# Performance work log

Hardware: AMD Instinct MI355X
Metric: run time of the kernel (lower is better)

## Reference

```python
import jax, jax.numpy as jnp
import numpy as np

D_MODEL = 1024
NUM_HEADS = 16
D_K = D_MODEL // NUM_HEADS
B, S = 2, 2048
LN_EPS = 1e-5


def setup_inputs() -> dict:
    key = jax.random.key(0)
    ks = jax.random.split(key, 11)
    sc = 1.0 / np.sqrt(D_MODEL)
    return {
        "x": jax.random.normal(ks[0], (B, S, D_MODEL), dtype=jnp.float32),
        "Wq": jax.random.normal(ks[1], (D_MODEL, D_MODEL), dtype=jnp.float32) * sc,
        "bq": jnp.zeros((D_MODEL,), dtype=jnp.float32),
        "Wk": jax.random.normal(ks[2], (D_MODEL, D_MODEL), dtype=jnp.float32) * sc,
        "bk": jnp.zeros((D_MODEL,), dtype=jnp.float32),
        "Wv": jax.random.normal(ks[3], (D_MODEL, D_MODEL), dtype=jnp.float32) * sc,
        "bv": jnp.zeros((D_MODEL,), dtype=jnp.float32),
        "Wo": jax.random.normal(ks[4], (D_MODEL, D_MODEL), dtype=jnp.float32) * sc,
        "bo": jnp.zeros((D_MODEL,), dtype=jnp.float32),
        "ln_gamma": jnp.ones((D_MODEL,), dtype=jnp.float32),
        "ln_beta": jnp.zeros((D_MODEL,), dtype=jnp.float32),
    }


def reference(x, Wq, bq, Wk, bk, Wv, bv, Wo, bo, ln_gamma, ln_beta):
    b, s, d = x.shape
    # QKV projections -> [B, H, S, D_K]
    def split_heads(y):
        return y.reshape(b, s, NUM_HEADS, D_K).transpose(0, 2, 1, 3)
    q = split_heads(x @ Wq + bq)
    k = split_heads(x @ Wk + bk)
    v = split_heads(x @ Wv + bv)
    # scores [B, H, S, S]; dropout is identity in eval mode
    scores = jnp.einsum("bhqd,bhkd->bhqk", q, k) / jnp.sqrt(jnp.float32(D_K))
    attn = jax.nn.softmax(scores, axis=-1)
    context = jnp.einsum("bhqk,bhkd->bhqd", attn, v)
    context = context.transpose(0, 2, 1, 3).reshape(b, s, d)
    out = context @ Wo + bo
    # residual + LayerNorm (eps=1e-5, torch default)
    h = x + out
    mu = jnp.mean(h, axis=-1, keepdims=True)
    var = jnp.var(h, axis=-1, keepdims=True)
    return (h - mu) / jnp.sqrt(var + LN_EPS) * ln_gamma + ln_beta
```

## Files before the change

kernel.cpp:

```cpp
#include <hip/hip_runtime.h>
#include <math.h>

#define D_MODEL 1024
#define NHEAD   16
#define DKK     64
#define BATCH   2
#define SEQ     2048
#define MROWS   (BATCH*SEQ)

typedef __attribute__((ext_vector_type(8)))  short bf16x8;
typedef __attribute__((ext_vector_type(4)))  short bf16x4;
typedef __attribute__((ext_vector_type(4)))  float f32x4;
typedef __attribute__((ext_vector_type(16))) float f32x16;

#define MFMA(a,b,c)   __builtin_amdgcn_mfma_f32_16x16x32_bf16((a),(b),(c),0,0,0)
#define MFMA32(a,b,c) __builtin_amdgcn_mfma_f32_32x32x16_bf16((a),(b),(c),0,0,0)

#define QSCALE 0.18033688f

#define SBAR() { __builtin_amdgcn_sched_barrier(0); \
                 __builtin_amdgcn_s_barrier();      \
                 __builtin_amdgcn_sched_barrier(0); }

#define CH  520
#define TIL (8*CH)

__device__ __forceinline__ short f2b(float f) {
    unsigned u = __float_as_uint(f);
    unsigned r = (u + 0x7FFFu + ((u >> 16) & 1u)) >> 16;
    return (short)r;
}
__device__ __forceinline__ float b2f(short s) {
    return __uint_as_float(((unsigned)(unsigned short)s) << 16);
}

__device__ __forceinline__ float fexp2(float x) {
    float r; asm("v_exp_f32 %0, %1" : "=v"(r) : "v"(x)); return r;
}

__device__ __forceinline__ void gld_lds16(const void* g, void* l) {
    __builtin_amdgcn_global_load_lds(
        (const __attribute__((address_space(1))) void*)g,
        (__attribute__((address_space(3))) void*)l, 16, 0, 0);
}

__global__ __launch_bounds__(256)
void prep_all(const float* __restrict__ x,
              const float* __restrict__ Wq, const float* __restrict__ Wk,
              const float* __restrict__ Wv, const float* __restrict__ Wo,
              short* __restrict__ xb, short* __restrict__ wt3,
              short* __restrict__ wot)
{
    const int z = blockIdx.z;
    if (z < 4) {
        const float* W = z==0 ? Wq : z==1 ? Wk : z==2 ? Wv : Wo;
        short* dst = (z < 3) ? (wt3 + (size_t)z*1024*1024) : wot;
        __shared__ float tile[32][33];
        const int tx = threadIdx.x & 31, ty = threadIdx.x >> 5;
        const int c0 = blockIdx.x*32, r0 = blockIdx.y*32;
        #pragma unroll
        for (int i = 0; i < 4; i++)
            tile[ty + i*8][tx] = W[(size_t)(r0 + ty + i*8)*1024 + c0 + tx];
        __syncthreads();
        #pragma unroll
        for (int i = 0; i < 4; i++)
            dst[(size_t)(c0 + ty + i*8)*1024 + r0 + tx] = f2b(tile[tx][ty + i*8]);
    } else {
        const int blk = (z-4)*1024 + blockIdx.y*32 + blockIdx.x;
        const int i = (blk*256 + threadIdx.x) * 8;
        float4 a = *(const float4*)(x + i);
        float4 c = *(const float4*)(x + i + 4);
        bf16x8 v;
        v[0]=f2b(a.x); v[1]=f2b(a.y); v[2]=f2b(a.z); v[3]=f2b(a.w);
        v[4]=f2b(c.x); v[5]=f2b(c.y); v[6]=f2b(c.z); v[7]=f2b(c.w);
        *(bf16x8*)(xb + i) = v;
    }
}

__global__ __launch_bounds__(512, 2)
void gemm_qkv(const short* __restrict__ A, const short* __restrict__ Bt,
              const float* __restrict__ bq, const float* __restrict__ bk,
              const float* __restrict__ bv,
              short* __restrict__ qb, short* __restrict__ kb, short* __restrict__ vtb)
{
    __shared__ short Ab[2*16384];
    __shared__ short Bb[2*12288];

    const int t = threadIdx.x;
    const int w = t >> 6, lane = t & 63;
    const int r = lane & 15, g4 = lane >> 4;
    const int wm = w >> 2, wn = w & 3;

    const int bid = blockIdx.x;
    const int xcd = bid & 7, idx = bid >> 3;
    const int mi  = (xcd >> 1) * 4 + (idx & 3);
    const int ni  = (xcd & 1) * 8 + (idx >> 2);
    const int m0 = mi * 256, n0 = ni * 192;

    const int srow = t >> 3;
    const int scol = ((t & 7) ^ (srow & 7)) * 8;

    f32x4 acc[8][3] = {};
    bf16x8 bfr[2][3];

#define QKV_STAGE(P, KT)                                                      \
    { const int kk = (KT) * 64 + scol;                                        \
      _Pragma("unroll")                                                       \
      for (int a = 0; a < 4; a++)                                             \
          gld_lds16(A + (size_t)(m0 + a*64 + srow)*1024 + kk,                 \
                    Ab + (P)*16384 + a*4096 + t*8);                           \
      _Pragma("unroll")                                                       \
      for (int p2 = 0; p2 < 3; p2++)                                          \
          gld_lds16(Bt + (size_t)(n0 + p2*64 + srow)*1024 + kk,               \
                    Bb + (P)*12288 + p2*4096 + t*8); }

#define QKV_PHASE2(P, MH)                                                     \
    { const short* Abase = Ab + (P)*16384 + wm*8192;                          \
      bf16x8 af[2][4];                                                        \
      _Pragma("unroll")                                                       \
      for (int ks = 0; ks < 2; ks++)                                          \
          _Pragma("unroll")                                                   \
          for (int i = 0; i < 4; i++)                                         \
              af[ks][i] = *(const bf16x8*)&Abase[((MH)*64 + i*16 + r)*64 +    \
                                                 ((ks*4 + g4) ^ (r&7))*8];    \
      if ((MH) == 0) {                                                        \
          const short* Bbase = Bb + (P)*12288;                                \
          _Pragma("unroll")                                                   \
          for (int ks = 0; ks < 2; ks++)                                      \
              _Pragma("unroll")                                               \
              for (int j = 0; j < 3; j++)                                     \
                  bfr[ks][j] = *(const bf16x8*)&Bbase[(wn*48 + j*16 + r)*64 + \
                                                      ((ks*4 + g4) ^ (r&7))*8]; \
      }                                                                       \
      __builtin_amdgcn_s_setprio(1);                                          \
      _Pragma("unroll")                                                       \
      for (int ks = 0; ks < 2; ks++)                                          \
          _Pragma("unroll")                                                   \
          for (int i = 0; i < 4; i++)                                         \
              _Pragma("unroll")                                               \
              for (int j = 0; j < 3; j++)                                     \
                  acc[(MH)*4+i][j] = MFMA(af[ks][i], bfr[ks][j],              \
                                          acc[(MH)*4+i][j]);                  \
      __builtin_amdgcn_s_setprio(0); }

    QKV_STAGE(0, 0)
    QKV_STAGE(1, 1)
    asm volatile("s_waitcnt vmcnt(7)" ::: "memory");
    __builtin_amdgcn_s_barrier();
    __builtin_amdgcn_sched_barrier(0);

    int p = 0;
    #pragma unroll 1
    for (int kt = 0; kt < 16; kt++) {
        QKV_PHASE2(p, 0)
        QKV_PHASE2(p, 1)
        SBAR();
        if (kt < 14) {
            QKV_STAGE(p, kt + 2)
            asm volatile("s_waitcnt vmcnt(7)" ::: "memory");
        } else {
            asm volatile("s_waitcnt vmcnt(0)" ::: "memory");
        }
        __builtin_amdgcn_s_barrier();
        __builtin_amdgcn_sched_barrier(0);
        p ^= 1;
    }
#undef QKV_STAGE
#undef QKV_PHASE2

    const int src4 = ((((lane & 3) << 4) | (lane >> 2)) << 2);
    const int dl   = lane >> 2;
    const int sl   = (lane & 3) * 4;

    #pragma unroll
    for (int n = 0; n < 3; n++) {
        const int colbase = n0 + wn*48 + n*16;
        const int proj    = colbase >> 10;
        const int within  = colbase & 1023;
        const int h       = within >> 6;
        const int d       = (within & 63) + r;
        const float* bias = (proj == 0) ? bq : (proj == 1) ? bk : bv;
        const float bval  = bias[within + r];
        #pragma unroll
        for (int m = 0; m < 8; m++) {
            const int growb = m0 + wm*128 + m*16 + g4*4;
            const int bidx  = growb >> 11;
            const int s     = growb & 2047;
            if (proj == 0) {
                #pragma unroll
                for (int i = 0; i < 4; i++)
                    qb[((size_t)(bidx*NHEAD + h)*SEQ + s + i)*DKK + d] =
                        f2b((acc[m][n][i] + bval) * QSCALE);
            } else if (proj == 1) {
                #pragma unroll
                for (int i = 0; i < 4; i++)
                    kb[((size_t)(bidx*NHEAD + h)*SEQ + s + i)*DKK + d] =
                        f2b(acc[m][n][i] + bval);
            } else {
                const int sbase = m0 + wm*128 + m*16;
                const int bidx2 = sbase >> 11;
                const int srw   = sbase & 2047;
                unsigned lo  = ((unsigned)(unsigned short)f2b(acc[m][n][1]+bval) << 16)
                             |  (unsigned)(unsigned short)f2b(acc[m][n][0]+bval);
                unsigned hi2 = ((unsigned)(unsigned short)f2b(acc[m][n][3]+bval) << 16)
                             |  (unsigned)(unsigned short)f2b(acc[m][n][2]+bval);
                unsigned t0 = (unsigned)__builtin_amdgcn_ds_bpermute(src4, (int)lo);
                unsigned t1 = (unsigned)__builtin_amdgcn_ds_bpermute(src4, (int)hi2);
                union { unsigned u[2]; bf16x4 v; } pk4;
                pk4.u[0] = t0; pk4.u[1] = t1;
                *(bf16x4*)(vtb + ((size_t)(bidx2*NHEAD + h)*DKK + (within & 63) + dl)*SEQ
                               + srw + sl) = pk4.v;
            }
        }
    }
}

__global__ __launch_bounds__(256)
void gemm_out(const short* __restrict__ A, const short* __restrict__ Bt,
              const float* __restrict__ bo, const short* __restrict__ resid,
              short* __restrict__ hb)
{
    __shared__ short As[2*128*32];
    __shared__ short Bs[2*64*32];
    const int t = threadIdx.x;
    const int w = t >> 6, lane = t & 63;
    const int r = lane & 15, g4 = lane >> 4;
    const int wr = w >> 1, wc = w & 1;

    const int bid = blockIdx.x;
    const int xcd = bid & 7, idx = bid >> 3;
    const int mi  = (xcd >> 1) * 8 + (idx & 7);
    const int ni  = (xcd & 1) * 8 + (idx >> 3);
    const int m0 = mi * 128, n0 = ni * 64;

    const int srow = lane >> 2, su = lane & 3;

    f32x4 acc[4][2] = {};

#define OUT_STAGE(BUF, K0)                                                     \
    { const int kk = (K0) & 1023;                                              \
      _Pragma("unroll")                                                        \
      for (int c = 0; c < 2; c++) {                                            \
          const int row = w*32 + c*16 + srow;                                  \
          gld_lds16(A + (size_t)(m0+row)*1024 + kk + 8*(su ^ ((row>>1)&3)),    \
                    As + (BUF)*4096 + w*1024 + c*512);                         \
      }                                                                        \
      { const int row = w*16 + srow;                                           \
        gld_lds16(Bt + (size_t)(n0+row)*1024 + kk + 8*(su ^ ((row>>1)&3)),     \
                  Bs + (BUF)*2048 + w*512); } }

    OUT_STAGE(0, 0)
    __syncthreads();

    int cur = 0;
    #pragma unroll 1
    for (int k0 = 0; k0 < 1024; k0 += 32) {
        OUT_STAGE(cur^1, k0 + 32)
        const short* Abase = As + cur*4096;
        const short* Bbase = Bs + cur*2048;
        bf16x8 af[4], bfr[2];
        #pragma unroll
        for (int m = 0; m < 4; m++) {
            const int row = wr*64 + m*16 + r;
            af[m] = *(const bf16x8*)&Abase[row*32 + (g4 ^ ((row>>1)&3))*8];
        }
        #pragma unroll
        for (int n = 0; n < 2; n++) {
            const int row = wc*32 + n*16 + r;
            bfr[n] = *(const bf16x8*)&Bbase[row*32 + (g4 ^ ((row>>1)&3))*8];
        }
        __builtin_amdgcn_s_setprio(1);
        #pragma unroll
        for (int m = 0; m < 4; m++)
            #pragma unroll
            for (int n = 0; n < 2; n++)
                acc[m][n] = MFMA(af[m], bfr[n], acc[m][n]);
        __builtin_amdgcn_s_setprio(0);
        __syncthreads();
        cur ^= 1;
    }
#undef OUT_STAGE

    #pragma unroll
    for (int n = 0; n < 2; n++) {
        const int col = n0 + wc*32 + n*16 + r;
        const float bval = bo[col];
        #pragma unroll
        for (int m = 0; m < 4; m++) {
            #pragma unroll
            for (int i = 0; i < 4; i++) {
                const int grow = m0 + wr*64 + m*16 + g4*4 + i;
                const size_t ofs = (size_t)grow*1024 + col;
                hb[ofs] = f2b(acc[m][n][i] + bval + b2f(resid[ofs]));
            }
        }
    }
}

__global__ __launch_bounds__(256, 2)
void attn_mfma(const short* __restrict__ Q, const short* __restrict__ K,
               const short* __restrict__ VT, short* __restrict__ ctx)
{
    __shared__ short Ks[4*TIL];
    __shared__ short Vs[4*TIL];

    const int t = threadIdx.x;
    const int w = t >> 6, lane = t & 63;
    const int l31 = lane & 31, hi = lane >> 5;
    const int srow8 = lane >> 3, su = lane & 7;
    const int lane8 = lane * 8;
    const int swz8  = (su ^ srow8) * 8;

    const int bid     = blockIdx.x;
    const int logical = (bid & 7) * 64 + (bid >> 3);
    const int bh_lin  = logical >> 4;
    const int qt      = logical & 15;
    const int b = bh_lin >> 4, h = bh_lin & 15;
    const int q0 = qt * 128 + w * 32;

    const size_t bh = (size_t)b * NHEAD + h;
    const short* Qp = Q  + bh * SEQ * DKK;
    const short* Kp = K  + bh * SEQ * DKK;
    const short* Vp = VT + bh * DKK * SEQ;

    const short* kstage = Kp + (size_t)(w*8 + srow8) * DKK + swz8;
    const short* vstage = Vp + (size_t)(w*8 + srow8) * SEQ + swz8;

    bf16x8 qf[4];
    #pragma unroll
    for (int d0 = 0; d0 < 4; d0++)
        qf[d0] = *(const bf16x8*)(Qp + (size_t)(q0 + l31)*DKK + d0*16 + hi*8);

    int koff[8], voff[8];
    #pragma unroll
    for (int i = 0; i < 8; i++) {
        const int kchunk = (i>>2)*4 + (l31>>3);
        koff[i] = kchunk*CH + (l31&7)*64 + ((((i&3)*2 + hi) ^ (l31&7)) * 8);
        const int vchunk = (i&1)*4 + (l31>>3);
        voff[i] = vchunk*CH + (l31&7)*64 + ((((i>>1)*2 + hi) ^ (l31&7)) * 8);
    }

    f32x16 o0A = {}, o1A = {}, o0B = {}, o1B = {}, lacc = {};

#define ATT_STAGE(KDST, VDST, J)                                               \
    { const size_t jj = (size_t)((J) & (SEQ-1));                               \
      const short* ksrc = kstage + jj*DKK;                                     \
      gld_lds16(ksrc,           (KDST) + w*CH + lane8);                        \
      gld_lds16(ksrc + 32*DKK,  (KDST) + (4+w)*CH + lane8);                    \
      const short* vsrc = vstage + jj;                                         \
      gld_lds16(vsrc,           (VDST) + w*CH + lane8);                        \
      gld_lds16(vsrc + 32*SEQ,  (VDST) + (4+w)*CH + lane8); }

#define QK_SUB(KB, S0, S1)                                                     \
    { bf16x8 kf[8];                                                            \
      _Pragma("unroll")                                                        \
      for (int i = 0; i < 8; i++) kf[i] = *(const bf16x8*)&(KB)[koff[i]];      \
      _Pragma("unroll")                                                        \
      for (int d0 = 0; d0 < 4; d0++) S0 = MFMA32(kf[d0],   qf[d0], S0);        \
      _Pragma("unroll")                                                        \
      for (int d0 = 0; d0 < 4; d0++) S1 = MFMA32(kf[4+d0], qf[d0], S1); }

#define PV_SUB(S0, S1, VB, O0, O1)                                             \
    { bf16x8 vf[8];                                                            \
      _Pragma("unroll")                                                        \
      for (int i = 0; i < 8; i++) vf[i] = *(const bf16x8*)&(VB)[voff[i]];      \
      _Pragma("unroll")                                                        \
      for (int ks = 0; ks < 4; ks++) {                                         \
        const int g = (ks & 1) * 8;                                            \
        float e0,e1,e2,e3,e4,e5,e6,e7;                                         \
        if (ks < 2) { e0=S0[g+0];e1=S0[g+1];e2=S0[g+2];e3=S0[g+3];             \
                      e4=S0[g+4];e5=S0[g+5];e6=S0[g+6];e7=S0[g+7]; }           \
        else        { e0=S1[g+0];e1=S1[g+1];e2=S1[g+2];e3=S1[g+3];             \
                      e4=S1[g+4];e5=S1[g+5];e6=S1[g+6];e7=S1[g+7]; }           \
        unsigned u0,u1,u2,u3;                                                  \
        asm("v_cvt_pk_bf16_f32 %0, %1, %2" : "=v"(u0) : "v"(e0), "v"(e1));     \
        asm("v_cvt_pk_bf16_f32 %0, %1, %2" : "=v"(u1) : "v"(e2), "v"(e3));     \
        asm("v_cvt_pk_bf16_f32 %0, %1, %2" : "=v"(u2) : "v"(e4), "v"(e5));     \
        asm("v_cvt_pk_bf16_f32 %0, %1, %2" : "=v"(u3) : "v"(e6), "v"(e7));     \
        auto rA = __builtin_amdgcn_permlane32_swap(u0, u2, false, false);      \
        auto rB = __builtin_amdgcn_permlane32_swap(u1, u3, false, false);      \
        union { unsigned u[4]; bf16x8 v; } pa;                                 \
        pa.u[0] = rA[0]; pa.u[1] = rB[0]; pa.u[2] = rA[1]; pa.u[3] = rB[1];    \
        O0 = MFMA32(pa.v, vf[ks*2+0], O0);                                     \
        O1 = MFMA32(pa.v, vf[ks*2+1], O1);                                     \
      } }

    ATT_STAGE(Ks,       Vs,       0)
    ATT_STAGE(Ks + TIL, Vs + TIL, 64)
    __syncthreads();

    int cur = 0;
    #pragma unroll 1
    for (int j0 = 0; j0 < SEQ; j0 += 128) {
        {
            const int nb = (cur^1)*2*TIL;
            ATT_STAGE(Ks + nb,       Vs + nb,       j0 + 128)
            ATT_STAGE(Ks + nb + TIL, Vs + nb + TIL, j0 + 192)
        }

        const short* KbA = Ks + cur*2*TIL;
        const short* VbA = Vs + cur*2*TIL;
        const short* KbB = KbA + TIL;
        const short* VbB = VbA + TIL;

        f32x16 s0A = {}, s1A = {}, s0B = {}, s1B = {};
        QK_SUB(KbA, s0A, s1A)
        QK_SUB(KbB, s0B, s1B)

        #pragma unroll
        for (int r = 0; r < 16; r++) s0A[r] = fexp2(s0A[r]);
        #pragma unroll
        for (int r = 0; r < 16; r++) s1A[r] = fexp2(s1A[r]);
        #pragma unroll
        for (int r = 0; r < 16; r++) s0B[r] = fexp2(s0B[r]);
        #pragma unroll
        for (int r = 0; r < 16; r++) s1B[r] = fexp2(s1B[r]);

        #pragma unroll
        for (int r = 0; r < 16; r++)
            lacc[r] += (s0A[r] + s1A[r]) + (s0B[r] + s1B[r]);

        PV_SUB(s0A, s1A, VbA, o0A, o1A)
        PV_SUB(s0B, s1B, VbB, o0B, o1B)

        __syncthreads();
        cur ^= 1;
    }

    float ts[16];
    #pragma unroll
    for (int r = 0; r < 16; r++) ts[r] = lacc[r];
    #pragma unroll
    for (int dd = 8; dd >= 1; dd >>= 1)
        #pragma unroll
        for (int r = 0; r < dd; r++) ts[r] += ts[r + dd];
    const float lrow = ts[0] + __shfl_xor(ts[0], 32);

    const float li = 1.f / lrow;
    const int lb = __float_as_int(li);
    #pragma unroll
    for (int r = 0; r < 16; r++) {
        const int crow = (r&3) + 8*(r>>2) + 4*hi;
        const float lv = __int_as_float(__builtin_amdgcn_ds_bpermute(crow*4, lb));
        const size_t base = ((size_t)b*SEQ + q0 + crow)*D_MODEL + h*DKK + l31;
        ctx[base]      = f2b((o0A[r] + o0B[r]) * lv);
        ctx[base + 32] = f2b((o1A[r] + o1B[r]) * lv);
    }
#undef ATT_STAGE
#undef QK_SUB
#undef PV_SUB
}

__global__ __launch_bounds__(256)
void ln_kernel(const short* __restrict__ hbuf, const float* __restrict__ gamma,
               const float* __restrict__ beta, float* __restrict__ out)
{
    const int row = blockIdx.x;
    const int t = threadIdx.x;
    const short* hp = hbuf + (size_t)row * D_MODEL;
    bf16x4 hv = ((const bf16x4*)hp)[t];
    float v0 = b2f(hv[0]), v1 = b2f(hv[1]), v2 = b2f(hv[2]), v3 = b2f(hv[3]);
    float sum = v0 + v1 + v2 + v3;
    float sq  = v0*v0 + v1*v1 + v2*v2 + v3*v3;
    #pragma unroll
    for (int o = 1; o <= 32; o <<= 1) {
        sum += __shfl_xor(sum, o);
        sq  += __shfl_xor(sq, o);
    }
    __shared__ float s1[4], s2[4];
    if ((t & 63) == 0) { s1[t >> 6] = sum; s2[t >> 6] = sq; }
    __syncthreads();
    sum = s1[0] + s1[1] + s1[2] + s1[3];
    sq  = s2[0] + s2[1] + s2[2] + s2[3];
    const float mean = sum * (1.0f / D_MODEL);
    const float var  = sq * (1.0f / D_MODEL) - mean * mean;
    const float inv  = rsqrtf(var + 1e-5f);
    float4 g  = ((const float4*)gamma)[t];
    float4 be = ((const float4*)beta)[t];
    float4 rr;
    rr.x = (v0 - mean) * inv * g.x + be.x;
    rr.y = (v1 - mean) * inv * g.y + be.y;
    rr.z = (v2 - mean) * inv * g.z + be.z;
    rr.w = (v3 - mean) * inv * g.w + be.w;
    ((float4*)(out + (size_t)row * D_MODEL))[t] = rr;
}

extern "C" void kernel_launch(void* const* d_in, const int* in_sizes, int n_in,
                              void* d_out, int out_size, void* d_ws, size_t ws_size,
                              hipStream_t stream)
{
    const float* x  = (const float*)d_in[0];
    const float* Wq = (const float*)d_in[1];
    const float* bq = (const float*)d_in[2];
    const float* Wk = (const float*)d_in[3];
    const float* bk = (const float*)d_in[4];
    const float* Wv = (const float*)d_in[5];
    const float* bv = (const float*)d_in[6];
    const float* Wo = (const float*)d_in[7];
    const float* bo = (const float*)d_in[8];
    const float* g  = (const float*)d_in[9];
    const float* be = (const float*)d_in[10];

    char* base = (char*)d_ws;
    short* xb   = (short*)base;
    short* wt3  = (short*)(base + (8u<<20));
    short* wot  = (short*)(base + (14u<<20));
    short* qb   = (short*)(base + (16u<<20));
    short* kb   = (short*)(base + (24u<<20));
    short* vtb  = (short*)(base + (32u<<20));
    short* cxb  = (short*)(base + (40u<<20));
    short* hb16 = (short*)(base + (48u<<20));

    prep_all  <<<dim3(32,32,6), 256, 0, stream>>>(x, Wq, Wk, Wv, Wo, xb, wt3, wot);
    gemm_qkv  <<<256, 512, 0, stream>>>(xb, wt3, bq, bk, bv, qb, kb, vtb);
    attn_mfma <<<512, 256, 0, stream>>>(qb, kb, vtb, cxb);
    gemm_out  <<<512, 256, 0, stream>>>(cxb, wot, bo, xb, hb16);
    ln_kernel <<<MROWS, 256, 0, stream>>>(hb16, g, be, (float*)d_out);
}
```

Before: 114.8 us.

## Deepen out-projection GEMM pipeline with BK=64 tiles and two-stage prefetch

Restructures the output-projection GEMM to load 64-wide K tiles with an XOR swizzle over 8 chunks. Two stages are kept in flight, with explicit vmcnt waits in place of a full sync after each 32-wide step. This halves the number of loop iterations and barriers and lets global loads overlap more compute, at the cost of doubling LDS use for this kernel. Only the gemm_out kernel changes; the attention and LayerNorm stages are untouched.

```diff
diff --git a/kernel.cpp b/kernel.cpp
--- a/kernel.cpp
+++ b/kernel.cpp
@@ -220,8 +220,8 @@
               const float* __restrict__ bo, const short* __restrict__ resid,
               short* __restrict__ hb)
 {
-    __shared__ short As[2*128*32];
-    __shared__ short Bs[2*64*32];
+    __shared__ short As[2*8192];
+    __shared__ short Bs[2*4096];
     const int t = threadIdx.x;
     const int w = t >> 6, lane = t & 63;
     const int r = lane & 15, g4 = lane >> 4;
@@ -233,53 +233,76 @@
     const int ni  = (xcd & 1) * 8 + (idx >> 3);
     const int m0 = mi * 128, n0 = ni * 64;
 
-    const int srow = lane >> 2, su = lane & 3;
+    const int srow = t >> 3;
+    const int scol = ((t & 7) ^ (srow & 7)) * 8;
 
     f32x4 acc[4][2] = {};
-
-#define OUT_STAGE(BUF, K0)                                                     \
-    { const int kk = (K0) & 1023;                                              \
-      _Pragma("unroll")                                                        \
-      for (int c = 0; c < 2; c++) {                                            \
-          const int row = w*32 + c*16 + srow;                                  \
-          gld_lds16(A + (size_t)(m0+row)*1024 + kk + 8*(su ^ ((row>>1)&3)),    \
-                    As + (BUF)*4096 + w*1024 + c*512);                         \
+    bf16x8 bfr[2][2];
+
+#define OUT_STAGE(P, KT)                                                       \
+    { const int kk = (KT) * 64 + scol;                                         \
+      _Pragma("unroll")                                                        \
+      for (int a = 0; a < 4; a++)                                              \
+          gld_lds16(A + (size_t)(m0 + a*32 + srow)*1024 + kk,                  \
+                    As + (P)*8192 + a*2048 + t*8);                             \
+      _Pragma("unroll")                                                        \
+      for (int b2 = 0; b2 < 2; b2++)                                           \
+          gld_lds16(Bt + (size_t)(n0 + b2*32 + srow)*1024 + kk,                \
+                    Bs + (P)*4096 + b2*2048 + t*8); }
+
+#define OUT_PHASE2(P, MH)                                                      \
+    { const short* Abase = As + (P)*8192 + wr*4096;                            \
+      bf16x8 af[2][2];                                                         \
+      _Pragma("unroll")                                                        \
+      for (int ks = 0; ks < 2; ks++)                                           \
+          _Pragma("unroll")                                                    \
+          for (int i = 0; i < 2; i++)                                          \
+              af[ks][i] = *(const bf16x8*)&Abase[((MH)*32 + i*16 + r)*64 +     \
+                                                 ((ks*4 + g4) ^ (r&7))*8];     \
+      if ((MH) == 0) {                                                         \
+          const short* Bbase = Bs + (P)*4096;                                  \
+          _Pragma("unroll")                                                    \
+          for (int ks = 0; ks < 2; ks++)                                       \
+              _Pragma("unroll")                                                \
+              for (int j = 0; j < 2; j++)                                      \
+                  bfr[ks][j] = *(const bf16x8*)&Bbase[(wc*32 + j*16 + r)*64 +  \
+                                                      ((ks*4 + g4) ^ (r&7))*8];\
       }                                                                        \
-      { const int row = w*16 + srow;                                           \
-        gld_lds16(Bt + (size_t)(n0+row)*1024 + kk + 8*(su ^ ((row>>1)&3)),     \
-                  Bs + (BUF)*2048 + w*512); } }
+      __builtin_amdgcn_s_setprio(1);                                           \
+      _Pragma("unroll")                                                        \
+      for (int ks = 0; ks < 2; ks++)                                           \
+          _Pragma("unroll")                                                    \
+          for (int i = 0; i < 2; i++)                                          \
+              _Pragma("unroll")                                                \
+              for (int j = 0; j < 2; j++)                                      \
+                  acc[(MH)*2+i][j] = MFMA(af[ks][i], bfr[ks][j],               \
+                                          acc[(MH)*2+i][j]);                   \
+      __builtin_amdgcn_s_setprio(0); }
 
     OUT_STAGE(0, 0)
-    __syncthreads();
-
-    int cur = 0;
+    OUT_STAGE(1, 1)
+    asm volatile("s_waitcnt vmcnt(6)" ::: "memory");
+    __builtin_amdgcn_s_barrier();
+    __builtin_amdgcn_sched_barrier(0);
+
+    int p = 0;
     #pragma unroll 1
-    for (int k0 = 0; k0 < 1024; k0 += 32) {
-        OUT_STAGE(cur^1, k0 + 32)
-        const short* Abase = As + cur*4096;
-        const short* Bbase = Bs + cur*2048;
-        bf16x8 af[4], bfr[2];
-        #pragma unroll
-        for (int m = 0; m < 4; m++) {
-            const int row = wr*64 + m*16 + r;
-            af[m] = *(const bf16x8*)&Abase[row*32 + (g4 ^ ((row>>1)&3))*8];
+    for (int kt = 0; kt < 16; kt++) {
+        OUT_PHASE2(p, 0)
+        OUT_PHASE2(p, 1)
+        SBAR();
+        if (kt < 14) {
+            OUT_STAGE(p, kt + 2)
+            asm volatile("s_waitcnt vmcnt(6)" ::: "memory");
+        } else {
+            asm volatile("s_waitcnt vmcnt(0)" ::: "memory");
         }
-        #pragma unroll
-        for (int n = 0; n < 2; n++) {
-            const int row = wc*32 + n*16 + r;
-            bfr[n] = *(const bf16x8*)&Bbase[row*32 + (g4 ^ ((row>>1)&3))*8];
-        }
-        __builtin_amdgcn_s_setprio(1);
-        #pragma unroll
-        for (int m = 0; m < 4; m++)
-            #pragma unroll
-            for (int n = 0; n < 2; n++)
-                acc[m][n] = MFMA(af[m], bfr[n], acc[m][n]);
-        __builtin_amdgcn_s_setprio(0);
-        __syncthreads();
-        cur ^= 1;
+        __builtin_amdgcn_s_barrier();
+        __builtin_amdgcn_sched_barrier(0);
+        p ^= 1;
     }
 #undef OUT_STAGE
+#undef OUT_PHASE2
 
     #pragma unroll
     for (int n = 0; n < 2; n++) {
```

New measurement: 111.4 us. -3.0%, faster.
